# Kernel tuning notes

Measured on AMD Instinct MI355X. Metric: run time of the kernel, lower is better.

The kernel has to match this reference:

```python
import jax, jax.numpy as jnp
import numpy as np

B, H, W, C = 4, 128, 128, 512
HID, HEADS, BS = 768, 8, 8
NBH, NBW = H // BS, W // BS
NBT, BS2 = NBH * NBW, BS * BS
HD = HID // HEADS


def setup_inputs() -> dict:
    key = jax.random.key(0)
    k = jax.random.split(key, 5)
    x = jax.random.normal(k[0], (B, H, W, C), jnp.float32)
    # attn weights must sum to 1 over the last dim
    attn_weights = jax.nn.softmax(
        jax.random.normal(k[1], (HEADS, B, NBT, BS2, BS2), jnp.float32), axis=-1)
    reordered_indexes = jnp.arange(H * W, dtype=jnp.int32).reshape(1, H * W, 1)
    W_in = jax.random.normal(k[2], (C, 3 * HID), jnp.float32) * (C ** -0.5)
    b_in = jnp.zeros((3 * HID,), jnp.float32)
    W_out = jax.random.normal(k[3], (HID, C), jnp.float32) * 0.05 * (HID ** -0.5)
    b_out = jnp.zeros((C,), jnp.float32)
    return dict(x=x, attn_weights=attn_weights, W_in=W_in, b_in=b_in,
                W_out=W_out, b_out=b_out, reordered_indexes=reordered_indexes)


def reference(x, attn_weights, W_in, b_in, W_out, b_out, reordered_indexes):
    idx = reordered_indexes.reshape(-1)  # (H*W,) permutation shared across batch
    # gather / token reorder
    x = x.reshape(B, H * W, C)[:, idx, :].reshape(B, H, W, C)
    # in_proj + split into (s, v, y); Balancer/Whiten/Identity are identity in fwd
    p = x @ W_in + b_in  # (B,H,W,3*HID)
    s, v, y = jnp.split(p, 3, axis=-1)
    v = v * jnp.tanh(s)
    # to per-block head layout: (heads, B, num_block_tot, bs^2, head_dim)
    v = v.reshape(B, NBH, BS, NBW, BS, HEADS, HD)
    v = v.transpose(5, 0, 1, 3, 2, 4, 6).reshape(HEADS, B, NBT, BS2, HD)
    v = jnp.einsum('hbnij,hbnjd->hbnid', attn_weights, v)
    # back to (B,H,W,HID)
    v = v.reshape(HEADS, B, NBH, NBW, BS, BS, HD)
    v = v.transpose(1, 2, 4, 3, 5, 0, 6).reshape(B, H, W, HID)
    out = (v * y) @ W_out + b_out  # (B,H,W,C)
    # scatter back to original token order
    out = out.reshape(B, H * W, C)
    out = jnp.zeros_like(out).at[:, idx, :].set(out)
    return out.reshape(B, H, W, C)
```

## Files before the change

### kernel.cpp

```cpp
#include <hip/hip_runtime.h>
#include <cstdint>
#include <cstddef>

#define Bb     4
#define Cc     512
#define HID    768
#define HEADS  8
#define NBT    256
#define BS2    64
#define HD     96
#define HWTOK  16384
#define MTOK   65536
#define N3     2304

typedef __attribute__((ext_vector_type(8))) short frag16;
typedef __attribute__((ext_vector_type(4))) float f32x4;

__device__ __forceinline__ float b2f(unsigned short u) {
    union { unsigned int i; float f; } x; x.i = ((unsigned int)u) << 16; return x.f;
}
__device__ __forceinline__ unsigned short f2b(float f) {
    union { float f; unsigned int i; } x; x.f = f;
    unsigned int r = x.i + 0x7fffu + ((x.i >> 16) & 1u);
    return (unsigned short)(r >> 16);
}
union cvt8 { uint4 u; unsigned short s[8]; };

__device__ __forceinline__ void gl2lds16(const void* g, void* l) {
    __builtin_amdgcn_global_load_lds(
        (const __attribute__((address_space(1))) unsigned int*)g,
        (__attribute__((address_space(3))) unsigned int*)l, 16, 0, 0);
}

__device__ __forceinline__ float fast_tanh(float x) {
    float a = __builtin_fabsf(x);
    float t = __expf(-2.0f * a);
    float r = (1.0f - t) / (1.0f + t);
    return __builtin_copysignf(r, x);
}

__global__ __launch_bounds__(256) void k_transpose(
    const float* __restrict__ w, unsigned short* __restrict__ wt,
    int K, int N) {
    int e = blockIdx.x * 256 + threadIdx.x;
    if (e < K * N) {
        int k = e / N, n = e - k * N;
        wt[(size_t)n * K + k] = f2b(w[e]);
    }
}

__global__ __launch_bounds__(256) void k_gather(
    const float* __restrict__ x, const int* __restrict__ idx,
    unsigned short* __restrict__ xg) {
    int gid = blockIdx.x * 256 + threadIdx.x;
    int t = gid >> 6, col = (gid & 63) * 8;
    int bb = t >> 14, hw = t & 16383;
    const float* src = x + ((size_t)bb * HWTOK + idx[hw]) * Cc + col;
    float4 f0 = *(const float4*)src, f1 = *(const float4*)(src + 4);
    cvt8 c;
    c.s[0] = f2b(f0.x); c.s[1] = f2b(f0.y); c.s[2] = f2b(f0.z); c.s[3] = f2b(f0.w);
    c.s[4] = f2b(f1.x); c.s[5] = f2b(f1.y); c.s[6] = f2b(f1.z); c.s[7] = f2b(f1.w);
    *(uint4*)(xg + (size_t)t * Cc + col) = c.u;
}

__global__ __launch_bounds__(256) void k_inproj(
    const unsigned short* __restrict__ xg,
    const unsigned short* __restrict__ winT,
    const float* __restrict__ b_in,
    unsigned short* __restrict__ y_img,
    unsigned short* __restrict__ vt_blk) {
    __shared__ alignas(16) unsigned short smem[2][10240];
    const int tid = threadIdx.x;
    const int wv = tid >> 6, lane = tid & 63;
    const int wm = wv >> 1, wn = wv & 1;
    const int fr = lane & 15, q = lane >> 4;

    const int fb = blockIdx.x + 12 * blockIdx.y;
    const int sb = (fb & 7) * 768 + (fb >> 3);
    const int n0 = (sb % 12) * 64;
    const int m0 = (sb / 12) * 128;

    const unsigned short* gsrc[5];
    int loff[5];
    #pragma unroll
    for (int ci = 0; ci < 5; ci++) {
        int c = wv * 5 + ci;
        if (c < 8) {
            gsrc[ci] = xg + (size_t)(m0 + c * 16 + fr) * Cc + q * 8;
            loff[ci] = c * 512;
        } else {
            int cb = c - 8, sl = cb >> 2;
            gsrc[ci] = winT + (size_t)(sl * HID + n0 + (cb & 3) * 16 + fr) * Cc + q * 8;
            loff[ci] = 4096 + cb * 512;
        }
    }

    f32x4 acc[3][2][4];
    #pragma unroll
    for (int sl = 0; sl < 3; sl++)
        #pragma unroll
        for (int nt = 0; nt < 2; nt++)
            #pragma unroll
            for (int mt = 0; mt < 4; mt++) acc[sl][nt][mt] = (f32x4){0.f,0.f,0.f,0.f};

    #pragma unroll
    for (int ci = 0; ci < 5; ci++) gl2lds16(gsrc[ci], &smem[0][loff[ci]]);

    #pragma unroll
    for (int t = 0; t < 16; t++) {
        if (t < 15) {
            #pragma unroll
            for (int ci = 0; ci < 5; ci++)
                gl2lds16(gsrc[ci] + (t + 1) * 32, &smem[(t + 1) & 1][loff[ci]]);
            asm volatile("s_waitcnt vmcnt(5)" ::: "memory");
        } else {
            asm volatile("s_waitcnt vmcnt(0)" ::: "memory");
        }
        __builtin_amdgcn_s_barrier();
        const unsigned short* sa = smem[t & 1];
        frag16 af[4];
        #pragma unroll
        for (int mt = 0; mt < 4; mt++)
            af[mt] = *(const frag16*)(sa + (wm * 4 + mt) * 512 + lane * 8);
        __builtin_amdgcn_s_setprio(1);
        #pragma unroll
        for (int sl = 0; sl < 3; sl++) {
            #pragma unroll
            for (int nt = 0; nt < 2; nt++) {
                frag16 bf = *(const frag16*)(sa + 4096 +
                                             (sl * 4 + wn * 2 + nt) * 512 + lane * 8);
                #pragma unroll
                for (int mt = 0; mt < 4; mt++)
                    acc[sl][nt][mt] = __builtin_amdgcn_mfma_f32_16x16x32_bf16(
                        af[mt], bf, acc[sl][nt][mt], 0, 0, 0);
            }
        }
        __builtin_amdgcn_s_setprio(0);
    }

    #pragma unroll
    for (int nt = 0; nt < 2; nt++) {
        const int j = n0 + wn * 32 + nt * 16 + fr;
        const float bs = b_in[j], bv = b_in[HID + j], by = b_in[2 * HID + j];
        const int h = j / HD, d = j - h * HD;
        #pragma unroll
        for (int mt = 0; mt < 4; mt++) {
            #pragma unroll
            for (int r = 0; r < 4; r++) {
                const int t = m0 + wm * 64 + mt * 16 + q * 4 + r;
                const int bb = t >> 14, hw = t & 16383;
                const float sv = acc[0][nt][mt][r] + bs;
                const float vv = acc[1][nt][mt][r] + bv;
                const float yv = acc[2][nt][mt][r] + by;
                y_img[(size_t)t * HID + j] = f2b(yv);
                const int hr = hw >> 7, wc = hw & 127;
                const int nblk = ((hr >> 3) << 4) | (wc >> 3);
                const int ii   = ((hr & 7) << 3) | (wc & 7);
                vt_blk[((((size_t)h * Bb + bb) * NBT + nblk) * BS2 + ii) * HD + d] =
                    f2b(vv * fast_tanh(sv));
            }
        }
    }
}

__global__ __launch_bounds__(256) void k_attn(
    const float* __restrict__ attnw,
    const unsigned short* __restrict__ vt_blk,
    unsigned short* __restrict__ y_img) {
    __shared__ alignas(16) unsigned short Aat[64][72];
    __shared__ alignas(16) unsigned short VtT[96][72];
    const int tid = threadIdx.x;
    const int g = blockIdx.x;
    const int wv = tid >> 6, lane = tid & 63;
    const int fr = lane & 15, q = lane >> 4;
    const int wm = wv >> 1, wn = wv & 1;

    const float* asrc = attnw + (size_t)g * 4096;
    const unsigned short* vsrc = vt_blk + (size_t)g * 6144;
    #pragma unroll
    for (int r = 0; r < 2; r++) {
        int v = tid + 256 * r;
        int i = v >> 3, jj = (v & 7) * 8;
        const float* ap = asrc + (size_t)v * 8;
        float4 f0 = *(const float4*)ap, f1 = *(const float4*)(ap + 4);
        cvt8 c;
        c.s[0]=f2b(f0.x); c.s[1]=f2b(f0.y); c.s[2]=f2b(f0.z); c.s[3]=f2b(f0.w);
        c.s[4]=f2b(f1.x); c.s[5]=f2b(f1.y); c.s[6]=f2b(f1.z); c.s[7]=f2b(f1.w);
        *(uint4*)(&Aat[i][jj]) = c.u;
    }
    #pragma unroll
    for (int r = 0; r < 3; r++) {
        int v = tid + 256 * r;
        int j = v / 12, dq = v - j * 12;
        cvt8 c; c.u = ((const uint4*)vsrc)[v];
        #pragma unroll
        for (int e = 0; e < 8; e++) VtT[dq * 8 + e][j] = c.s[e];
    }
    __syncthreads();

    f32x4 acc[2][3];
    #pragma unroll
    for (int mt = 0; mt < 2; mt++)
        #pragma unroll
        for (int nd = 0; nd < 3; nd++) acc[mt][nd] = (f32x4){0.f,0.f,0.f,0.f};
    #pragma unroll
    for (int kk = 0; kk < 2; kk++) {
        frag16 af[2];
        #pragma unroll
        for (int mt = 0; mt < 2; mt++)
            af[mt] = *(const frag16*)(&Aat[wm * 32 + mt * 16 + fr][kk * 32 + q * 8]);
        #pragma unroll
        for (int nd = 0; nd < 3; nd++) {
            frag16 bf = *(const frag16*)(&VtT[wn * 48 + nd * 16 + fr][kk * 32 + q * 8]);
            #pragma unroll
            for (int mt = 0; mt < 2; mt++)
                acc[mt][nd] = __builtin_amdgcn_mfma_f32_16x16x32_bf16(
                    af[mt], bf, acc[mt][nd], 0, 0, 0);
        }
    }

    const int h = g >> 10, b = (g >> 8) & 3, n = g & 255;
    #pragma unroll
    for (int nd = 0; nd < 3; nd++) {
        const int d = wn * 48 + nd * 16 + fr;
        #pragma unroll
        for (int mt = 0; mt < 2; mt++) {
            #pragma unroll
            for (int r = 0; r < 4; r++) {
                const int i = wm * 32 + mt * 16 + q * 4 + r;
                const int hr = ((n >> 4) << 3) | (i >> 3);
                const int wc = ((n & 15) << 3) | (i & 7);
                const size_t t = ((size_t)b << 14) + (size_t)hr * 128 + wc;
                const size_t off = t * HID + (size_t)h * HD + d;
                y_img[off] = f2b(acc[mt][nd][r] * b2f(y_img[off]));
            }
        }
    }
}

__global__ __launch_bounds__(256) void k_outproj(
    const unsigned short* __restrict__ avy,
    const unsigned short* __restrict__ woutT,
    const float* __restrict__ b_out,
    const int* __restrict__ idx,
    float* __restrict__ out) {
    __shared__ alignas(16) unsigned short smem[2][8192];
    const int tid = threadIdx.x;
    const int wv = tid >> 6, lane = tid & 63;
    const int wm = wv >> 1, wn = wv & 1;
    const int fr = lane & 15, q = lane >> 4;

    const int fb = blockIdx.x + 4 * blockIdx.y;
    const int sb = (fb & 7) * 256 + (fb >> 3);
    const int c0 = (sb % 4) * 128;
    const int m0 = (sb / 4) * 128;

    const unsigned short* gsrc[4];
    int loff[4];
    #pragma unroll
    for (int ci = 0; ci < 4; ci++) {
        int c = wv * 4 + ci;
        if (c < 8) {
            gsrc[ci] = avy + (size_t)(m0 + c * 16 + fr) * HID + q * 8;
            loff[ci] = c * 512;
        } else {
            int cb = c - 8;
            gsrc[ci] = woutT + (size_t)(c0 + cb * 16 + fr) * HID + q * 8;
            loff[ci] = 4096 + cb * 512;
        }
    }

    f32x4 acc[4][4];
    #pragma unroll
    for (int nt = 0; nt < 4; nt++)
        #pragma unroll
        for (int mt = 0; mt < 4; mt++) acc[nt][mt] = (f32x4){0.f,0.f,0.f,0.f};

    #pragma unroll
    for (int ci = 0; ci < 4; ci++) gl2lds16(gsrc[ci], &smem[0][loff[ci]]);

    #pragma unroll
    for (int t = 0; t < 24; t++) {
        if (t < 23) {
            #pragma unroll
            for (int ci = 0; ci < 4; ci++)
                gl2lds16(gsrc[ci] + (t + 1) * 32, &smem[(t + 1) & 1][loff[ci]]);
            asm volatile("s_waitcnt vmcnt(4)" ::: "memory");
        } else {
            asm volatile("s_waitcnt vmcnt(0)" ::: "memory");
        }
        __builtin_amdgcn_s_barrier();
        const unsigned short* sa = smem[t & 1];
        frag16 af[4];
        #pragma unroll
        for (int mt = 0; mt < 4; mt++)
            af[mt] = *(const frag16*)(sa + (wm * 4 + mt) * 512 + lane * 8);
        __builtin_amdgcn_s_setprio(1);
        #pragma unroll
        for (int nt = 0; nt < 4; nt++) {
            frag16 bf = *(const frag16*)(sa + 4096 + (wn * 4 + nt) * 512 + lane * 8);
            #pragma unroll
            for (int mt = 0; mt < 4; mt++)
                acc[nt][mt] = __builtin_amdgcn_mfma_f32_16x16x32_bf16(
                    af[mt], bf, acc[nt][mt], 0, 0, 0);
        }
        __builtin_amdgcn_s_setprio(0);
    }

    #pragma unroll
    for (int nt = 0; nt < 4; nt++) {
        const int c = c0 + wn * 64 + nt * 16 + fr;
        const float bo = b_out[c];
        #pragma unroll
        for (int mt = 0; mt < 4; mt++) {
            #pragma unroll
            for (int r = 0; r < 4; r++) {
                const int t = m0 + wm * 64 + mt * 16 + q * 4 + r;
                const int bb = t >> 14, hw = t & 16383;
                const int dst = idx[hw];
                out[((size_t)bb * HWTOK + dst) * Cc + c] = acc[nt][mt][r] + bo;
            }
        }
    }
}

extern "C" void kernel_launch(void* const* d_in, const int* in_sizes, int n_in,
                              void* d_out, int out_size, void* d_ws, size_t ws_size,
                              hipStream_t stream) {
    const float* x     = (const float*)d_in[0];
    const float* attnw = (const float*)d_in[1];
    const float* W_in  = (const float*)d_in[2];
    const float* b_in  = (const float*)d_in[3];
    const float* W_out = (const float*)d_in[4];
    const float* b_out = (const float*)d_in[5];
    const int*   idx   = (const int*)d_in[6];
    float*       out   = (float*)d_out;

    char* p = (char*)d_ws;
    unsigned short* winT  = (unsigned short*)p; p += (size_t)N3 * Cc * 2;
    unsigned short* woutT = (unsigned short*)p; p += (size_t)Cc * HID * 2;
    unsigned short* vt    = (unsigned short*)p; p += (size_t)HEADS * Bb * NBT * BS2 * HD * 2;
    unsigned short* y_img = (unsigned short*)p; p += (size_t)MTOK * HID * 2;
    unsigned short* xg = (unsigned short*)d_out;

    k_transpose<<<(N3 * Cc + 255) / 256, 256, 0, stream>>>(W_in, winT, Cc, N3);
    k_transpose<<<(HID * Cc + 255) / 256, 256, 0, stream>>>(W_out, woutT, HID, Cc);
    k_gather<<<MTOK * 64 / 256, 256, 0, stream>>>(x, idx, xg);

    dim3 g1(HID / 64, MTOK / 128);
    k_inproj<<<g1, 256, 0, stream>>>(xg, winT, b_in, y_img, vt);

    k_attn<<<HEADS * Bb * NBT, 256, 0, stream>>>(attnw, vt, y_img);

    dim3 g3(Cc / 128, MTOK / 128);
    k_outproj<<<g3, 256, 0, stream>>>(y_img, woutT, b_out, idx, out);
}
```

Baseline: 756.5 us.

## Load GEMM B fragments directly from global into registers, triple-buffer A in LDS

In both the in-projection and out-projection GEMMs, the weight (B) tiles are no longer staged through LDS. Each wave now loads its B fragments straight from global memory into double-buffered registers. Only the activation (A) tiles still go through LDS, which moves from two buffers to three, and the vmcnt wait counts are adjusted to match. The aim is to cut LDS traffic and footprint, which may raise occupancy, at the cost of more VGPRs and duplicated B reads across the two wm waves.

```diff
diff --git a/kernel.cpp b/kernel.cpp
--- a/kernel.cpp
+++ b/kernel.cpp
@@ -69,7 +69,7 @@
     const float* __restrict__ b_in,
     unsigned short* __restrict__ y_img,
     unsigned short* __restrict__ vt_blk) {
-    __shared__ alignas(16) unsigned short smem[2][10240];
+    __shared__ alignas(16) unsigned short smem[3][4096];
     const int tid = threadIdx.x;
     const int wv = tid >> 6, lane = tid & 63;
     const int wm = wv >> 1, wn = wv & 1;
@@ -80,20 +80,21 @@
     const int n0 = (sb % 12) * 64;
     const int m0 = (sb / 12) * 128;
 
-    const unsigned short* gsrc[5];
-    int loff[5];
-    #pragma unroll
-    for (int ci = 0; ci < 5; ci++) {
-        int c = wv * 5 + ci;
-        if (c < 8) {
-            gsrc[ci] = xg + (size_t)(m0 + c * 16 + fr) * Cc + q * 8;
-            loff[ci] = c * 512;
-        } else {
-            int cb = c - 8, sl = cb >> 2;
-            gsrc[ci] = winT + (size_t)(sl * HID + n0 + (cb & 3) * 16 + fr) * Cc + q * 8;
-            loff[ci] = 4096 + cb * 512;
-        }
-    }
+    const unsigned short* ga[2];
+    int la[2];
+    #pragma unroll
+    for (int ci = 0; ci < 2; ci++) {
+        int c = wv * 2 + ci;
+        ga[ci] = xg + (size_t)(m0 + c * 16 + fr) * Cc + q * 8;
+        la[ci] = c * 512;
+    }
+    const unsigned short* bsrc[6];
+    #pragma unroll
+    for (int sl = 0; sl < 3; sl++)
+        #pragma unroll
+        for (int nt = 0; nt < 2; nt++)
+            bsrc[sl * 2 + nt] = winT +
+                (size_t)(sl * HID + n0 + wn * 32 + nt * 16 + fr) * Cc + q * 8;
 
     f32x4 acc[3][2][4];
     #pragma unroll
@@ -103,21 +104,27 @@
             #pragma unroll
             for (int mt = 0; mt < 4; mt++) acc[sl][nt][mt] = (f32x4){0.f,0.f,0.f,0.f};
 
-    #pragma unroll
-    for (int ci = 0; ci < 5; ci++) gl2lds16(gsrc[ci], &smem[0][loff[ci]]);
+    frag16 bfb[2][6];
+    #pragma unroll
+    for (int ci = 0; ci < 2; ci++) gl2lds16(ga[ci], &smem[0][la[ci]]);
+    #pragma unroll
+    for (int i = 0; i < 6; i++) bfb[0][i] = *(const frag16*)(bsrc[i]);
 
     #pragma unroll
     for (int t = 0; t < 16; t++) {
         if (t < 15) {
             #pragma unroll
-            for (int ci = 0; ci < 5; ci++)
-                gl2lds16(gsrc[ci] + (t + 1) * 32, &smem[(t + 1) & 1][loff[ci]]);
-            asm volatile("s_waitcnt vmcnt(5)" ::: "memory");
+            for (int ci = 0; ci < 2; ci++)
+                gl2lds16(ga[ci] + (t + 1) * 32, &smem[(t + 1) % 3][la[ci]]);
+            #pragma unroll
+            for (int i = 0; i < 6; i++)
+                bfb[(t + 1) & 1][i] = *(const frag16*)(bsrc[i] + (t + 1) * 32);
+            asm volatile("s_waitcnt vmcnt(8)" ::: "memory");
         } else {
             asm volatile("s_waitcnt vmcnt(0)" ::: "memory");
         }
         __builtin_amdgcn_s_barrier();
-        const unsigned short* sa = smem[t & 1];
+        const unsigned short* sa = smem[t % 3];
         frag16 af[4];
         #pragma unroll
         for (int mt = 0; mt < 4; mt++)
@@ -127,8 +134,7 @@
         for (int sl = 0; sl < 3; sl++) {
             #pragma unroll
             for (int nt = 0; nt < 2; nt++) {
-                frag16 bf = *(const frag16*)(sa + 4096 +
-                                             (sl * 4 + wn * 2 + nt) * 512 + lane * 8);
+                frag16 bf = bfb[t & 1][sl * 2 + nt];
                 #pragma unroll
                 for (int mt = 0; mt < 4; mt++)
                     acc[sl][nt][mt] = __builtin_amdgcn_mfma_f32_16x16x32_bf16(
@@ -244,7 +250,7 @@
     const float* __restrict__ b_out,
     const int* __restrict__ idx,
     float* __restrict__ out) {
-    __shared__ alignas(16) unsigned short smem[2][8192];
+    __shared__ alignas(16) unsigned short smem[3][4096];
     const int tid = threadIdx.x;
     const int wv = tid >> 6, lane = tid & 63;
     const int wm = wv >> 1, wn = wv & 1;
@@ -255,20 +261,18 @@
     const int c0 = (sb % 4) * 128;
     const int m0 = (sb / 4) * 128;
 
-    const unsigned short* gsrc[4];
-    int loff[4];
-    #pragma unroll
-    for (int ci = 0; ci < 4; ci++) {
-        int c = wv * 4 + ci;
-        if (c < 8) {
-            gsrc[ci] = avy + (size_t)(m0 + c * 16 + fr) * HID + q * 8;
-            loff[ci] = c * 512;
-        } else {
-            int cb = c - 8;
-            gsrc[ci] = woutT + (size_t)(c0 + cb * 16 + fr) * HID + q * 8;
-            loff[ci] = 4096 + cb * 512;
-        }
-    }
+    const unsigned short* ga[2];
+    int la[2];
+    #pragma unroll
+    for (int ci = 0; ci < 2; ci++) {
+        int c = wv * 2 + ci;
+        ga[ci] = avy + (size_t)(m0 + c * 16 + fr) * HID + q * 8;
+        la[ci] = c * 512;
+    }
+    const unsigned short* bsrc[4];
+    #pragma unroll
+    for (int nt = 0; nt < 4; nt++)
+        bsrc[nt] = woutT + (size_t)(c0 + wn * 64 + nt * 16 + fr) * HID + q * 8;
 
     f32x4 acc[4][4];
     #pragma unroll
@@ -276,21 +280,27 @@
         #pragma unroll
         for (int mt = 0; mt < 4; mt++) acc[nt][mt] = (f32x4){0.f,0.f,0.f,0.f};
 
-    #pragma unroll
-    for (int ci = 0; ci < 4; ci++) gl2lds16(gsrc[ci], &smem[0][loff[ci]]);
+    frag16 bfb[2][4];
+    #pragma unroll
+    for (int ci = 0; ci < 2; ci++) gl2lds16(ga[ci], &smem[0][la[ci]]);
+    #pragma unroll
+    for (int i = 0; i < 4; i++) bfb[0][i] = *(const frag16*)(bsrc[i]);
 
     #pragma unroll
     for (int t = 0; t < 24; t++) {
         if (t < 23) {
             #pragma unroll
-            for (int ci = 0; ci < 4; ci++)
-                gl2lds16(gsrc[ci] + (t + 1) * 32, &smem[(t + 1) & 1][loff[ci]]);
-            asm volatile("s_waitcnt vmcnt(4)" ::: "memory");
+            for (int ci = 0; ci < 2; ci++)
+                gl2lds16(ga[ci] + (t + 1) * 32, &smem[(t + 1) % 3][la[ci]]);
+            #pragma unroll
+            for (int i = 0; i < 4; i++)
+                bfb[(t + 1) & 1][i] = *(const frag16*)(bsrc[i] + (t + 1) * 32);
+            asm volatile("s_waitcnt vmcnt(6)" ::: "memory");
         } else {
             asm volatile("s_waitcnt vmcnt(0)" ::: "memory");
         }
         __builtin_amdgcn_s_barrier();
-        const unsigned short* sa = smem[t & 1];
+        const unsigned short* sa = smem[t % 3];
         frag16 af[4];
         #pragma unroll
         for (int mt = 0; mt < 4; mt++)
@@ -298,7 +308,7 @@
         __builtin_amdgcn_s_setprio(1);
         #pragma unroll
         for (int nt = 0; nt < 4; nt++) {
-            frag16 bf = *(const frag16*)(sa + 4096 + (wn * 4 + nt) * 512 + lane * 8);
+            frag16 bf = bfb[t & 1][nt];
             #pragma unroll
             for (int mt = 0; mt < 4; mt++)
                 acc[nt][mt] = __builtin_amdgcn_mfma_f32_16x16x32_bf16(
```

New measurement: 892.7 us. 18.0% more time.

## Store y in per-block head layout and triple-buffer GEMM LDS stages

Applied to the files above, without the earlier changes.

The y projection is now written in the same blocked head layout as v, so the attention kernel reads it contiguously through LDS and writes v*y back in place instead of scattering into token order. The out-projection then computes per-token block addresses and walks the head stride as it steps through K. Both GEMM kernels also move from double to triple buffering in shared memory. The goal is coalesced access in the attention kernel, at the cost of strided A-tile loads in the out-projection and more LDS per block, which may lower occupancy.

```diff
diff --git a/kernel.cpp b/kernel.cpp
--- a/kernel.cpp
+++ b/kernel.cpp
@@ -12,6 +12,7 @@
 #define HWTOK  16384
 #define MTOK   65536
 #define N3     2304
+#define HSTR   ((size_t)Bb * NBT * BS2 * HD)
 
 typedef __attribute__((ext_vector_type(8))) short frag16;
 typedef __attribute__((ext_vector_type(4))) float f32x4;
@@ -37,6 +38,11 @@
     float t = __expf(-2.0f * a);
     float r = (1.0f - t) / (1.0f + t);
     return __builtin_copysignf(r, x);
+}
+
+__device__ __forceinline__ size_t aoff(int kt) {
+    const int k0 = kt * 32;
+    return (size_t)(k0 / HD) * HSTR + (size_t)(k0 % HD);
 }
 
 __global__ __launch_bounds__(256) void k_transpose(
@@ -67,9 +73,9 @@
     const unsigned short* __restrict__ xg,
     const unsigned short* __restrict__ winT,
     const float* __restrict__ b_in,
-    unsigned short* __restrict__ y_img,
+    unsigned short* __restrict__ y_blk,
     unsigned short* __restrict__ vt_blk) {
-    __shared__ alignas(16) unsigned short smem[2][10240];
+    __shared__ alignas(16) unsigned short smem[3][10240];
     const int tid = threadIdx.x;
     const int wv = tid >> 6, lane = tid & 63;
     const int wm = wv >> 1, wn = wv & 1;
@@ -111,13 +117,13 @@
         if (t < 15) {
             #pragma unroll
             for (int ci = 0; ci < 5; ci++)
-                gl2lds16(gsrc[ci] + (t + 1) * 32, &smem[(t + 1) & 1][loff[ci]]);
+                gl2lds16(gsrc[ci] + (t + 1) * 32, &smem[(t + 1) % 3][loff[ci]]);
             asm volatile("s_waitcnt vmcnt(5)" ::: "memory");
         } else {
             asm volatile("s_waitcnt vmcnt(0)" ::: "memory");
         }
         __builtin_amdgcn_s_barrier();
-        const unsigned short* sa = smem[t & 1];
+        const unsigned short* sa = smem[t % 3];
         frag16 af[4];
         #pragma unroll
         for (int mt = 0; mt < 4; mt++)
@@ -152,12 +158,13 @@
                 const float sv = acc[0][nt][mt][r] + bs;
                 const float vv = acc[1][nt][mt][r] + bv;
                 const float yv = acc[2][nt][mt][r] + by;
-                y_img[(size_t)t * HID + j] = f2b(yv);
                 const int hr = hw >> 7, wc = hw & 127;
                 const int nblk = ((hr >> 3) << 4) | (wc >> 3);
                 const int ii   = ((hr & 7) << 3) | (wc & 7);
-                vt_blk[((((size_t)h * Bb + bb) * NBT + nblk) * BS2 + ii) * HD + d] =
-                    f2b(vv * fast_tanh(sv));
+                const size_t boff =
+                    ((((size_t)h * Bb + bb) * NBT + nblk) * BS2 + ii) * HD + d;
+                y_blk[boff]  = f2b(yv);
+                vt_blk[boff] = f2b(vv * fast_tanh(sv));
             }
         }
     }
@@ -166,9 +173,10 @@
 __global__ __launch_bounds__(256) void k_attn(
     const float* __restrict__ attnw,
     const unsigned short* __restrict__ vt_blk,
-    unsigned short* __restrict__ y_img) {
+    unsigned short* y_blk) {
     __shared__ alignas(16) unsigned short Aat[64][72];
     __shared__ alignas(16) unsigned short VtT[96][72];
+    __shared__ alignas(16) unsigned short Yt[64 * 96];
     const int tid = threadIdx.x;
     const int g = blockIdx.x;
     const int wv = tid >> 6, lane = tid & 63;
@@ -177,6 +185,13 @@
 
     const float* asrc = attnw + (size_t)g * 4096;
     const unsigned short* vsrc = vt_blk + (size_t)g * 6144;
+    unsigned short* ysrc = y_blk + (size_t)g * 6144;
+
+    #pragma unroll
+    for (int r = 0; r < 3; r++) {
+        const int vb = wv * 64 + r * 256;
+        gl2lds16(ysrc + (size_t)(vb + lane) * 8, Yt + (size_t)vb * 8);
+    }
     #pragma unroll
     for (int r = 0; r < 2; r++) {
         int v = tid + 256 * r;
@@ -219,7 +234,6 @@
         }
     }
 
-    const int h = g >> 10, b = (g >> 8) & 3, n = g & 255;
     #pragma unroll
     for (int nd = 0; nd < 3; nd++) {
         const int d = wn * 48 + nd * 16 + fr;
@@ -228,11 +242,8 @@
             #pragma unroll
             for (int r = 0; r < 4; r++) {
                 const int i = wm * 32 + mt * 16 + q * 4 + r;
-                const int hr = ((n >> 4) << 3) | (i >> 3);
-                const int wc = ((n & 15) << 3) | (i & 7);
-                const size_t t = ((size_t)b << 14) + (size_t)hr * 128 + wc;
-                const size_t off = t * HID + (size_t)h * HD + d;
-                y_img[off] = f2b(acc[mt][nd][r] * b2f(y_img[off]));
+                const float yv = b2f(Yt[i * HD + d]);
+                ysrc[i * HD + d] = f2b(acc[mt][nd][r] * yv);
             }
         }
     }
@@ -244,7 +255,7 @@
     const float* __restrict__ b_out,
     const int* __restrict__ idx,
     float* __restrict__ out) {
-    __shared__ alignas(16) unsigned short smem[2][8192];
+    __shared__ alignas(16) unsigned short smem[3][8192];
     const int tid = threadIdx.x;
     const int wv = tid >> 6, lane = tid & 63;
     const int wm = wv >> 1, wn = wv & 1;
@@ -261,7 +272,12 @@
     for (int ci = 0; ci < 4; ci++) {
         int c = wv * 4 + ci;
         if (c < 8) {
-            gsrc[ci] = avy + (size_t)(m0 + c * 16 + fr) * HID + q * 8;
+            int tok = m0 + c * 16 + fr;
+            int bb = tok >> 14, hw = tok & 16383;
+            int hr = hw >> 7, wc = hw & 127;
+            int nblk = ((hr >> 3) << 4) | (wc >> 3);
+            int ii = ((hr & 7) << 3) | (wc & 7);
+            gsrc[ci] = avy + (((size_t)bb * NBT + nblk) * BS2 + ii) * HD + q * 8;
             loff[ci] = c * 512;
         } else {
             int cb = c - 8;
@@ -269,6 +285,7 @@
             loff[ci] = 4096 + cb * 512;
         }
     }
+    const bool waveA = (wv < 2);
 
     f32x4 acc[4][4];
     #pragma unroll
@@ -282,15 +299,16 @@
     #pragma unroll
     for (int t = 0; t < 24; t++) {
         if (t < 23) {
+            const size_t off = waveA ? aoff(t + 1) : (size_t)(t + 1) * 32;
             #pragma unroll
             for (int ci = 0; ci < 4; ci++)
-                gl2lds16(gsrc[ci] + (t + 1) * 32, &smem[(t + 1) & 1][loff[ci]]);
+                gl2lds16(gsrc[ci] + off, &smem[(t + 1) % 3][loff[ci]]);
             asm volatile("s_waitcnt vmcnt(4)" ::: "memory");
         } else {
             asm volatile("s_waitcnt vmcnt(0)" ::: "memory");
         }
         __builtin_amdgcn_s_barrier();
-        const unsigned short* sa = smem[t & 1];
+        const unsigned short* sa = smem[t % 3];
         frag16 af[4];
         #pragma unroll
         for (int mt = 0; mt < 4; mt++)
@@ -298,7 +316,8 @@
         __builtin_amdgcn_s_setprio(1);
         #pragma unroll
         for (int nt = 0; nt < 4; nt++) {
-            frag16 bf = *(const frag16*)(sa + 4096 + (wn * 4 + nt) * 512 + lane * 8);
+            frag16 bf = *(const frag16*)(sa + 4096 +
+                                         (wn * 4 + nt) * 512 + lane * 8);
             #pragma unroll
             for (int mt = 0; mt < 4; mt++)
                 acc[nt][mt] = __builtin_amdgcn_mfma_f32_16x16x32_bf16(
@@ -340,7 +359,7 @@
     unsigned short* winT  = (unsigned short*)p; p += (size_t)N3 * Cc * 2;
     unsigned short* woutT = (unsigned short*)p; p += (size_t)Cc * HID * 2;
     unsigned short* vt    = (unsigned short*)p; p += (size_t)HEADS * Bb * NBT * BS2 * HD * 2;
-    unsigned short* y_img = (unsigned short*)p; p += (size_t)MTOK * HID * 2;
+    unsigned short* y_blk = (unsigned short*)p; p += (size_t)HEADS * Bb * NBT * BS2 * HD * 2;
     unsigned short* xg = (unsigned short*)d_out;
 
     k_transpose<<<(N3 * Cc + 255) / 256, 256, 0, stream>>>(W_in, winT, Cc, N3);
@@ -348,10 +367,10 @@
     k_gather<<<MTOK * 64 / 256, 256, 0, stream>>>(x, idx, xg);
 
     dim3 g1(HID / 64, MTOK / 128);
-    k_inproj<<<g1, 256, 0, stream>>>(xg, winT, b_in, y_img, vt);
-
-    k_attn<<<HEADS * Bb * NBT, 256, 0, stream>>>(attnw, vt, y_img);
+    k_inproj<<<g1, 256, 0, stream>>>(xg, winT, b_in, y_blk, vt);
+
+    k_attn<<<HEADS * Bb * NBT, 256, 0, stream>>>(attnw, vt, y_blk);
 
     dim3 g3(Cc / 128, MTOK / 128);
-    k_outproj<<<g3, 256, 0, stream>>>(y_img, woutT, b_out, idx, out);
-}
+    k_outproj<<<g3, 256, 0, stream>>>(y_blk, woutT, b_out, idx, out);
+}
```

Measured after the change: 723.2 us. 4.4% less time.
